# Performance work log

Measured on AMD Instinct MI355X. Metric: run time of the kernel, lower is better.

The kernel has to match this reference:

```python
import jax, jax.numpy as jnp
import numpy as np

E = 16        # num_experts
TOPK = 2      # num_experts_per_tok


def setup_inputs() -> dict:
    key = jax.random.key(0)
    ks = jax.random.split(key, 8)
    B, S, H, I, IS = 4, 2048, 1024, 512, 2048
    std = 0.02
    return {
        "hidden_states": jax.random.normal(ks[0], (B, S, H), jnp.float32),
        "gate_w": jax.random.normal(ks[1], (E, H), jnp.float32) * std,
        "gate_up_proj": jax.random.normal(ks[2], (E, 2 * I, H), jnp.float32) * std,
        "down_proj": jax.random.normal(ks[3], (E, H, I), jnp.float32) * std,
        "shared_gate_proj": jax.random.normal(ks[4], (IS, H), jnp.float32) * std,
        "shared_up_proj": jax.random.normal(ks[5], (IS, H), jnp.float32) * std,
        "shared_down_proj": jax.random.normal(ks[6], (H, IS), jnp.float32) * std,
        "shared_expert_gate_w": jax.random.normal(ks[7], (1, H), jnp.float32) * std,
    }


def _moe(x, gate_w, gate_up_proj, down_proj, sgp, sup, sdp, segw):
    # x: [N, H] flattened tokens
    N = x.shape[0]
    router_logits = x @ gate_w.T                      # [N, E]
    probs = jax.nn.softmax(router_logits, axis=-1)
    routing_weights, selected = jax.lax.top_k(probs, TOPK)   # [N, TOPK]
    routing_weights = routing_weights / routing_weights.sum(-1, keepdims=True)
    # combine weights scattered into dense [N, E] (per-token per-expert gate)
    combine = jnp.zeros((N, E), x.dtype).at[jnp.arange(N)[:, None], selected].add(routing_weights)

    def body(acc, ws):
        gu_w, d_w, cw = ws                            # [2I,H], [H,I], [N]
        gu = x @ gu_w.T                               # [N, 2I]
        g, u = jnp.split(gu, 2, axis=-1)
        h = jax.nn.silu(g) * u                        # [N, I]
        return acc + cw[:, None] * (h @ d_w.T), None

    expert_out, _ = jax.lax.scan(body, jnp.zeros_like(x), (gate_up_proj, down_proj, combine.T))

    # shared expert with sigmoid token gate
    shared_h = jax.nn.silu(x @ sgp.T) * (x @ sup.T)   # [N, IS]
    shared_out = (shared_h @ sdp.T) * jax.nn.sigmoid(x @ segw.T)  # [N, H]
    out = expert_out + shared_out

    # aux (load-balancing) loss
    counts = jnp.sum(jax.nn.one_hot(selected, E, dtype=x.dtype), axis=(0, 1))  # [E]
    frac_tokens = counts / (N * TOPK)
    frac_probs = probs.sum(0) / N
    aux_loss = E * jnp.sum(frac_tokens * frac_probs)
    return out, aux_loss


def reference(hidden_states, gate_w, gate_up_proj, down_proj, shared_gate_proj, shared_up_proj, shared_down_proj, shared_expert_gate_w):
    B, S, H = hidden_states.shape
    out, aux = _moe(hidden_states.reshape(-1, H), gate_w, gate_up_proj, down_proj,
                    shared_gate_proj, shared_up_proj, shared_down_proj, shared_expert_gate_w)
    return out.reshape(B, S, H), aux
```

## Files before the change

### kernel.cpp

```cpp
#include <hip/hip_runtime.h>
#include <hip/hip_bf16.h>
#include <stdint.h>


#define N_TOK 8192
#define HDIM 1024
#define NEXP 16
#define IEXP 512
#define ISH 2048

typedef __bf16 bf16x8 __attribute__((ext_vector_type(8)));
typedef float f32x4 __attribute__((ext_vector_type(4)));

#define OFF_XBF   ((size_t)0)
#define OFF_WSG   ((size_t)16777216)
#define OFF_WSU   ((size_t)20971520)
#define OFF_WSD   ((size_t)25165824)
#define OFF_SH    ((size_t)29360128)
#define OFF_HEXP  ((size_t)62914560)
#define OFF_IDS   ((size_t)79691776)
#define OFF_META  ((size_t)80216064)
#define OFF_SIG   ((size_t)80216320)
#define OFF_LG    ((size_t)80249088)
#define OFF_SLOT  ((size_t)81297664)
#define OFF_TWAB  ((size_t)81363200)

#define WGU_NEW   ((size_t)81428736)
#define WDN_NEW   ((size_t)(WGU_NEW + 33554432))
#define NEED_FULL ((size_t)(WDN_NEW + 16777216))

static __device__ __forceinline__ unsigned short f2bf(float f) {
  unsigned int u = __float_as_uint(f);
  u += 0x7fffu + ((u >> 16) & 1u);
  return (unsigned short)(u >> 16);
}
static __device__ __forceinline__ int pack_bf2(float a, float b) {
  return (int)f2bf(a) | ((int)f2bf(b) << 16);
}
static __device__ __forceinline__ float bf2f(unsigned short u) {
  return __uint_as_float(((unsigned int)u) << 16);
}
static __device__ __forceinline__ void gl_lds16(const void* g, void* l) {
  __builtin_amdgcn_global_load_lds(
      (const __attribute__((address_space(1))) unsigned int*)g,
      (__attribute__((address_space(3))) unsigned int*)l, 16, 0, 0);
}

__global__ void cvt_kernel(const float* __restrict__ src,
                           unsigned short* __restrict__ dst, int n4) {
  int i = blockIdx.x * 256 + threadIdx.x;
  if (i >= n4) return;
  float4 v = ((const float4*)src)[i];
  uint2 o;
  o.x = (unsigned)pack_bf2(v.x, v.y);
  o.y = (unsigned)pack_bf2(v.z, v.w);
  ((uint2*)dst)[i] = o;
}

#define CV_WSG 524288
#define CV_WSU 1048576
#define CV_WSD 1572864
#define CV_WGU 5767168
#define CV_ALL 7864320
__global__ void cvt5_kernel(const float* __restrict__ WSG, const float* __restrict__ WSU,
                            const float* __restrict__ WSD, const float* __restrict__ WGU,
                            const float* __restrict__ WDN,
                            unsigned short* __restrict__ wsg, unsigned short* __restrict__ wsu,
                            unsigned short* __restrict__ wsd, unsigned short* __restrict__ wgu,
                            unsigned short* __restrict__ wdn) {
  int i = blockIdx.x * 256 + threadIdx.x;
  if (i >= CV_ALL) return;
  const float* src; unsigned short* dst; int k;
  if (i < CV_WSG)      { src = WSG; dst = wsg; k = i; }
  else if (i < CV_WSU) { src = WSU; dst = wsu; k = i - CV_WSG; }
  else if (i < CV_WSD) { src = WSD; dst = wsd; k = i - CV_WSU; }
  else if (i < CV_WGU) { src = WGU; dst = wgu; k = i - CV_WSD; }
  else                 { src = WDN; dst = wdn; k = i - CV_WGU; }
  float4 v = ((const float4*)src)[k];
  uint2 o;
  o.x = (unsigned)pack_bf2(v.x, v.y);
  o.y = (unsigned)pack_bf2(v.z, v.w);
  ((uint2*)dst)[k] = o;
}

__global__ __launch_bounds__(256) void logits_kernel(
    const float* __restrict__ X, const float* __restrict__ GW,
    const float* __restrict__ SEGW, float* __restrict__ LG,
    unsigned short* __restrict__ XBF) {
  int wid = threadIdx.x >> 6, lane = threadIdx.x & 63;
  int tok = blockIdx.x * 4 + wid;
  const float* xr = X + (size_t)tok * HDIM;
  unsigned short* xw = XBF + (size_t)tok * HDIM;
  float xv[16];
#pragma unroll
  for (int i = 0; i < 16; i++) xv[i] = xr[lane + 64 * i];
#pragma unroll
  for (int i = 0; i < 16; i++) xw[lane + 64 * i] = f2bf(xv[i]);
  float myv = 0.f;
#pragma unroll
  for (int e = 0; e < 17; e++) {
    const float* wr = (e < 16) ? (GW + (size_t)e * HDIM) : SEGW;
    float p = 0.f;
#pragma unroll
    for (int i = 0; i < 16; i++) p += xv[i] * wr[lane + 64 * i];
#pragma unroll
    for (int off = 32; off >= 1; off >>= 1) p += __shfl_xor(p, off, 64);
    if (lane == e) myv = p;
  }
  if (lane < 17) LG[(size_t)tok * 32 + lane] = myv;
}

__global__ __launch_bounds__(256) void route_kernel(
    const float* __restrict__ LG, int* __restrict__ cnt,
    float* __restrict__ pps, int* __restrict__ ids,
    int* __restrict__ slotAB, float* __restrict__ twAB,
    float* __restrict__ sig) {
  __shared__ int lcnt[16];
  __shared__ int lbase[16];
  __shared__ float lps[16];
  int tid = threadIdx.x;
  int tok = blockIdx.x * 256 + tid;
  if (tid < 16) { lcnt[tid] = 0; lps[tid] = 0.f; }
  __syncthreads();
  const float4* row = (const float4*)(LG + (size_t)tok * 32);
  float4 v0 = row[0], v1 = row[1], v2 = row[2], v3 = row[3];
  float g16 = row[4].x;
  float lg[16] = {v0.x, v0.y, v0.z, v0.w, v1.x, v1.y, v1.z, v1.w,
                  v2.x, v2.y, v2.z, v2.w, v3.x, v3.y, v3.z, v3.w};
  float mx = lg[0];
#pragma unroll
  for (int e = 1; e < 16; e++) mx = fmaxf(mx, lg[e]);
  float pr[16], s = 0.f;
#pragma unroll
  for (int e = 0; e < 16; e++) { pr[e] = __expf(lg[e] - mx); s += pr[e]; }
  float inv_s = 1.f / s;
  float p1 = -1.f, p2 = -1.f; int i1 = 0, i2 = 0;
#pragma unroll
  for (int e = 0; e < 16; e++) {
    if (pr[e] > p1) { p2 = p1; i2 = i1; p1 = pr[e]; i1 = e; }
    else if (pr[e] > p2) { p2 = pr[e]; i2 = e; }
  }
  float wsum = p1 + p2;
  int s1 = atomicAdd(&lcnt[i1], 1);
  int s2 = atomicAdd(&lcnt[i2], 1);
#pragma unroll
  for (int e = 0; e < 16; e++) atomicAdd(&lps[e], pr[e] * inv_s);
  sig[tok] = 1.f / (1.f + __expf(-g16));
  __syncthreads();
  if (tid < 16) {
    lbase[tid] = atomicAdd(&cnt[tid], lcnt[tid]);
    atomicAdd(&pps[tid], lps[tid]);
  }
  __syncthreads();
  int sl1 = lbase[i1] + s1, sl2 = lbase[i2] + s2;
  ids[i1 * N_TOK + sl1] = tok;
  ids[i2 * N_TOK + sl2] = tok;
  slotAB[tok * 2]     = (i1 << 14) | sl1;
  slotAB[tok * 2 + 1] = (i2 << 14) | sl2;
  twAB[tok * 2]     = p1 / wsum;
  twAB[tok * 2 + 1] = p2 / wsum;
}

__global__ void offs_aux_kernel(const int* __restrict__ cnt, int* __restrict__ off,
                                const float* __restrict__ probs_sum,
                                float* __restrict__ out_aux) {
  if (threadIdx.x == 0 && blockIdx.x == 0) {
    int run = 0; float aux = 0.f;
    for (int e = 0; e < NEXP; e++) {
      off[e] = run; run += cnt[e];
      aux += ((float)cnt[e] / (float)(N_TOK * 2)) * (probs_sum[e] / (float)N_TOK);
    }
    off[16] = run;
    *out_aux = (float)NEXP * aux;
  }
}

template <int TMODE>
__global__ __launch_bounds__(512, 2) void g8p_kernel(
    const unsigned short* __restrict__ A0,
    const unsigned short* __restrict__ Bg,
    const unsigned short* __restrict__ Bu,
    const unsigned short* __restrict__ Bgu,
    const unsigned short* __restrict__ Bd,
    const int* __restrict__ ids, const int* __restrict__ cnt,
    const int* __restrict__ off,
    unsigned short* __restrict__ Osh,
    unsigned short* __restrict__ Ohex,
    unsigned short* __restrict__ Oeout) {
  constexpr int KD = (TMODE == 2) ? IEXP : HDIM;
  constexpr int NK = KD / 64;
  extern __shared__ unsigned short lds[];

  int rmode, e = 0, bx, by, m0step;
  if constexpr (TMODE == 3) {
    int id = blockIdx.x;
    if (id < 512) { rmode = 0; bx = id & 15; by = id >> 4; m0step = 8192; }
    else {
      int id2 = id - 512;
      rmode = 1; e = id2 >> 5; bx = id2 & 3; by = (id2 >> 2) & 7; m0step = 2048;
    }
  } else if constexpr (TMODE == 0) {
    rmode = 0; bx = blockIdx.x; by = blockIdx.y; m0step = 8192;
  } else if constexpr (TMODE == 1) {
    rmode = 1; e = blockIdx.z; bx = blockIdx.x; by = blockIdx.y;
    m0step = (int)gridDim.y * 256;
  } else {
    rmode = 2; e = blockIdx.z; bx = blockIdx.x; by = blockIdx.y;
    m0step = (int)gridDim.y * 256;
  }

  int ne, base = 0;
  if (rmode == 0) { ne = N_TOK; }
  else { ne = cnt[e]; base = off[e]; }

  const int t = threadIdx.x, lane = t & 63, w = t >> 6;
  const int fr = lane & 15, hi = lane >> 4;
  const int rq = hi * 4;
  const int Rm = (w >> 2) * 64;
  const int wn = (w & 3) * 32;
  const int srow = t >> 3;
  const int sblk = t & 7;
  const int cb = (sblk ^ (srow & 7)) * 8;
  const int s0 = ((0 + hi) ^ (fr & 7)) * 8;
  const int s1 = ((4 + hi) ^ (fr & 7)) * 8;
  const f32x4 z4 = {0.f, 0.f, 0.f, 0.f};

#define STG_A(buf, h, kt)                                                     \
  do {                                                                        \
    gl_lds16(apt[h][0] + (kt) * 64, &lds[(buf)*32768 + (h)*8192 + t * 8]);    \
    gl_lds16(apt[h][1] + (kt) * 64,                                           \
             &lds[(buf)*32768 + (h)*8192 + 4096 + t * 8]);                    \
  } while (0)
#define STG_B(buf, h, kt)                                                     \
  do {                                                                        \
    gl_lds16(bpt[h][0] + (kt) * 64,                                           \
             &lds[(buf)*32768 + 16384 + (h)*8192 + t * 8]);                   \
    gl_lds16(bpt[h][1] + (kt) * 64,                                           \
             &lds[(buf)*32768 + 16384 + (h)*8192 + 4096 + t * 8]);            \
  } while (0)

  for (int m0 = by * 256; m0 < ne; m0 += m0step) {
    const unsigned short* apt[2][2];
    const unsigned short* bpt[2][2];
#pragma unroll
    for (int h = 0; h < 2; h++)
#pragma unroll
      for (int l = 0; l < 2; l++) {
        int r = h * 128 + l * 64 + srow;
        if (rmode == 0) {
          apt[h][l] = A0 + (size_t)(m0 + r) * HDIM + cb;
        } else if (rmode == 1) {
          int slot = m0 + r;
          int arow = (slot < ne) ? ids[e * N_TOK + slot] : 0;
          apt[h][l] = A0 + (size_t)arow * HDIM + cb;
        } else {
          int ra = base + m0 + r;
          if (ra > 16383) ra = 16383;
          apt[h][l] = A0 + (size_t)ra * IEXP + cb;
        }
        if (rmode == 0) {
          int gcol = bx * 128 + ((r >> 5) << 4) + (r & 15);
          const unsigned short* W = (r & 16) ? Bu : Bg;
          bpt[h][l] = W + (size_t)gcol * HDIM + cb;
        } else if (rmode == 1) {
          int wrow = ((r & 16) ? 512 : 0) + bx * 128 + ((r >> 5) << 4) + (r & 15);
          bpt[h][l] = Bgu + ((size_t)e * 1024 + wrow) * HDIM + cb;
        } else {
          int nrow = bx * 256 + r;
          bpt[h][l] = Bd + ((size_t)e * HDIM + nrow) * IEXP + cb;
        }
      }

    f32x4 acc[8][4];
#pragma unroll
    for (int i = 0; i < 8; i++)
#pragma unroll
      for (int j = 0; j < 4; j++) acc[i][j] = z4;

    STG_A(0, 0, 0); STG_B(0, 1, 0); STG_A(0, 1, 0); STG_B(0, 0, 0);
    STG_A(1, 0, 1); STG_B(1, 1, 1);
    asm volatile("s_waitcnt vmcnt(4)" ::: "memory");
    __builtin_amdgcn_s_barrier();

    for (int kt = 0; kt < NK; ++kt) {
      const int c = kt & 1, nb = c ^ 1;
      const unsigned short* Ab = &lds[c * 32768];
      const unsigned short* Bb = &lds[c * 32768 + 16384];
      bf16x8 a[4][2], b[2][2];

#pragma unroll
      for (int i = 0; i < 4; i++) {
        int ro = (Rm + i * 16 + fr) * 64;
        a[i][0] = *(const bf16x8*)&Ab[ro + s0];
        a[i][1] = *(const bf16x8*)&Ab[ro + s1];
      }
#pragma unroll
      for (int j = 0; j < 2; j++) {
        int ro = (wn + j * 16 + fr) * 64;
        b[j][0] = *(const bf16x8*)&Bb[ro + s0];
        b[j][1] = *(const bf16x8*)&Bb[ro + s1];
      }
      if (kt + 1 < NK) STG_A(nb, 1, kt + 1);
      __builtin_amdgcn_s_barrier();
      asm volatile("s_waitcnt lgkmcnt(0)" ::: "memory");
      __builtin_amdgcn_s_setprio(1);
#pragma unroll
      for (int i = 0; i < 4; i++)
#pragma unroll
        for (int j = 0; j < 2; j++) {
          acc[i][j] = __builtin_amdgcn_mfma_f32_16x16x32_bf16(a[i][0], b[j][0], acc[i][j], 0, 0, 0);
          acc[i][j] = __builtin_amdgcn_mfma_f32_16x16x32_bf16(a[i][1], b[j][1], acc[i][j], 0, 0, 0);
        }
      __builtin_amdgcn_s_setprio(0);
      __builtin_amdgcn_s_barrier();

#pragma unroll
      for (int j = 0; j < 2; j++) {
        int ro = (128 + wn + j * 16 + fr) * 64;
        b[j][0] = *(const bf16x8*)&Bb[ro + s0];
        b[j][1] = *(const bf16x8*)&Bb[ro + s1];
      }
      if (kt + 1 < NK) STG_B(nb, 0, kt + 1);
      __builtin_amdgcn_s_barrier();
      asm volatile("s_waitcnt lgkmcnt(0)" ::: "memory");
      __builtin_amdgcn_s_setprio(1);
#pragma unroll
      for (int i = 0; i < 4; i++)
#pragma unroll
        for (int j = 0; j < 2; j++) {
          acc[i][2 + j] = __builtin_amdgcn_mfma_f32_16x16x32_bf16(a[i][0], b[j][0], acc[i][2 + j], 0, 0, 0);
          acc[i][2 + j] = __builtin_amdgcn_mfma_f32_16x16x32_bf16(a[i][1], b[j][1], acc[i][2 + j], 0, 0, 0);
        }
      __builtin_amdgcn_s_setprio(0);
      __builtin_amdgcn_s_barrier();

#pragma unroll
      for (int i = 0; i < 4; i++) {
        int ro = (128 + Rm + i * 16 + fr) * 64;
        a[i][0] = *(const bf16x8*)&Ab[ro + s0];
        a[i][1] = *(const bf16x8*)&Ab[ro + s1];
      }
      if (kt + 2 < NK) STG_A(c, 0, kt + 2);
      __builtin_amdgcn_s_barrier();
      asm volatile("s_waitcnt lgkmcnt(0)" ::: "memory");
      __builtin_amdgcn_s_setprio(1);
#pragma unroll
      for (int i = 0; i < 4; i++)
#pragma unroll
        for (int j = 0; j < 2; j++) {
          acc[4 + i][2 + j] = __builtin_amdgcn_mfma_f32_16x16x32_bf16(a[i][0], b[j][0], acc[4 + i][2 + j], 0, 0, 0);
          acc[4 + i][2 + j] = __builtin_amdgcn_mfma_f32_16x16x32_bf16(a[i][1], b[j][1], acc[4 + i][2 + j], 0, 0, 0);
        }
      __builtin_amdgcn_s_setprio(0);
      __builtin_amdgcn_s_barrier();

#pragma unroll
      for (int j = 0; j < 2; j++) {
        int ro = (wn + j * 16 + fr) * 64;
        b[j][0] = *(const bf16x8*)&Bb[ro + s0];
        b[j][1] = *(const bf16x8*)&Bb[ro + s1];
      }
      if (kt + 2 < NK) STG_B(c, 1, kt + 2);
      __builtin_amdgcn_s_barrier();
      asm volatile("s_waitcnt lgkmcnt(0)" ::: "memory");
      __builtin_amdgcn_s_setprio(1);
#pragma unroll
      for (int i = 0; i < 4; i++)
#pragma unroll
        for (int j = 0; j < 2; j++) {
          acc[4 + i][j] = __builtin_amdgcn_mfma_f32_16x16x32_bf16(a[i][0], b[j][0], acc[4 + i][j], 0, 0, 0);
          acc[4 + i][j] = __builtin_amdgcn_mfma_f32_16x16x32_bf16(a[i][1], b[j][1], acc[4 + i][j], 0, 0, 0);
        }
      __builtin_amdgcn_s_setprio(0);
      if (kt + 2 < NK) asm volatile("s_waitcnt vmcnt(4)" ::: "memory");
      else             asm volatile("s_waitcnt vmcnt(0)" ::: "memory");
      __builtin_amdgcn_s_barrier();
    }

#pragma unroll
    for (int i = 0; i < 8; i++) {
      int mloc = (i >> 2) * 128 + Rm + (i & 3) * 16 + rq;
      if (rmode == 2) {
#pragma unroll
        for (int j = 0; j < 4; j++) {
          int nn = bx * 256 + (j >> 1) * 128 + wn + (j & 1) * 16 + fr;
#pragma unroll
          for (int r = 0; r < 4; r++) {
            int slot = m0 + mloc + r;
            if (slot < ne)
              Oeout[(size_t)(base + slot) * HDIM + nn] = f2bf(acc[i][j][r]);
          }
        }
      } else {
#pragma unroll
        for (int p = 0; p < 2; p++) {
          int cc = bx * 128 + p * 64 + (w & 3) * 16 + fr;
#pragma unroll
          for (int r = 0; r < 4; r++) {
            int slot = m0 + mloc + r;
            float g = acc[i][2 * p][r], u = acc[i][2 * p + 1][r];
            float hv = g / (1.f + __expf(-g)) * u;
            if (rmode == 0) {
              Osh[(size_t)slot * ISH + cc] = f2bf(hv);
            } else if (slot < ne) {
              Ohex[(size_t)(base + slot) * IEXP + cc] = f2bf(hv);
            }
          }
        }
      }
    }
  }
#undef STG_A
#undef STG_B
}

template <int FUSE>
__global__ __launch_bounds__(256) void sg2c_kernel(
    const unsigned short* __restrict__ H, const unsigned short* __restrict__ Wd,
    const float* __restrict__ sig, const unsigned short* __restrict__ Eout,
    const int* __restrict__ slotAB, const float* __restrict__ twAB,
    const int* __restrict__ off, float* __restrict__ Out) {
  __shared__ __align__(16) unsigned short As[128 * 32];
  __shared__ __align__(16) unsigned short Bs[128 * 32];
  int m0 = blockIdx.y * 128, n0 = blockIdx.x * 128;
  int t = threadIdx.x, lane = t & 63, w = t >> 6;
  int wm = (w & 1) * 64, wn = (w >> 1) * 64;
  int arow = t >> 2, akb = (t & 3) * 8;
  const unsigned short* apA0 = H + (size_t)(m0 + arow) * ISH + akb;
  const unsigned short* apA1 = H + (size_t)(m0 + 64 + arow) * ISH + akb;
  const unsigned short* apB0 = Wd + (size_t)(n0 + arow) * ISH + akb;
  const unsigned short* apB1 = Wd + (size_t)(n0 + 64 + arow) * ISH + akb;
  f32x4 z = {0.f, 0.f, 0.f, 0.f};
  f32x4 acc[4][4];
#pragma unroll
  for (int i = 0; i < 4; i++)
#pragma unroll
    for (int j = 0; j < 4; j++) acc[i][j] = z;
  for (int k0 = 0; k0 < ISH; k0 += 32) {
    __syncthreads();
    gl_lds16(apA0 + k0, &As[t * 8]);
    gl_lds16(apA1 + k0, &As[2048 + t * 8]);
    gl_lds16(apB0 + k0, &Bs[t * 8]);
    gl_lds16(apB1 + k0, &Bs[2048 + t * 8]);
    __syncthreads();
    int fr = lane & 15, fc = (lane >> 4) * 8;
    bf16x8 af[4], bfr[4];
#pragma unroll
    for (int i = 0; i < 4; i++) {
      af[i] = *(const bf16x8*)&As[(wm + i * 16 + fr) * 32 + fc];
      bfr[i] = *(const bf16x8*)&Bs[(wn + i * 16 + fr) * 32 + fc];
    }
#pragma unroll
    for (int i = 0; i < 4; i++)
#pragma unroll
      for (int j = 0; j < 4; j++)
        acc[i][j] = __builtin_amdgcn_mfma_f32_16x16x32_bf16(af[i], bfr[j], acc[i][j], 0, 0, 0);
  }
  int col = lane & 15, rq = (lane >> 4) * 4;
#pragma unroll
  for (int i = 0; i < 4; i++)
#pragma unroll
    for (int r = 0; r < 4; r++) {
      int mm = m0 + wm + i * 16 + rq + r;
      float sg = sig[mm];
      if (FUSE) {
        int sa = slotAB[mm * 2], sb = slotAB[mm * 2 + 1];
        float wa = twAB[mm * 2], wb = twAB[mm * 2 + 1];
        size_t ra = (size_t)(off[sa >> 14] + (sa & 16383)) * HDIM;
        size_t rb = (size_t)(off[sb >> 14] + (sb & 16383)) * HDIM;
#pragma unroll
        for (int j = 0; j < 4; j++) {
          int nn = n0 + wn + j * 16 + col;
          float ea = bf2f(Eout[ra + nn]);
          float eb = bf2f(Eout[rb + nn]);
          Out[(size_t)mm * HDIM + nn] = acc[i][j][r] * sg + wa * ea + wb * eb;
        }
      } else {
#pragma unroll
        for (int j = 0; j < 4; j++) {
          int nn = n0 + wn + j * 16 + col;
          Out[(size_t)mm * HDIM + nn] = acc[i][j][r] * sg;
        }
      }
    }
}

__global__ __launch_bounds__(256) void combine_kernel(
    const unsigned short* __restrict__ Eout, const int* __restrict__ slotAB,
    const float* __restrict__ twAB, const int* __restrict__ off,
    float* __restrict__ Out) {
  int tok = blockIdx.x, t = threadIdx.x;
  int sa = slotAB[tok * 2], sb = slotAB[tok * 2 + 1];
  float wa = twAB[tok * 2], wb = twAB[tok * 2 + 1];
  int ra = off[sa >> 14] + (sa & 16383);
  int rb = off[sb >> 14] + (sb & 16383);
  const ushort4 a4 = *(const ushort4*)(Eout + (size_t)ra * HDIM + t * 4);
  const ushort4 b4 = *(const ushort4*)(Eout + (size_t)rb * HDIM + t * 4);
  float* po = Out + (size_t)tok * HDIM + t * 4;
  float4 o = *(const float4*)po;
  o.x += wa * bf2f(a4.x) + wb * bf2f(b4.x);
  o.y += wa * bf2f(a4.y) + wb * bf2f(b4.y);
  o.z += wa * bf2f(a4.z) + wb * bf2f(b4.z);
  o.w += wa * bf2f(a4.w) + wb * bf2f(b4.w);
  *(float4*)po = o;
}

extern "C" void kernel_launch(void* const* d_in, const int* in_sizes, int n_in,
                              void* d_out, int out_size, void* d_ws, size_t ws_size,
                              hipStream_t stream) {
  const float* X   = (const float*)d_in[0];
  const float* GW  = (const float*)d_in[1];
  const float* WGU = (const float*)d_in[2];
  const float* WDN = (const float*)d_in[3];
  const float* WSG = (const float*)d_in[4];
  const float* WSU = (const float*)d_in[5];
  const float* WSD = (const float*)d_in[6];
  const float* SEGW = (const float*)d_in[7];
  float* Out = (float*)d_out;
  char* ws = (char*)d_ws;

  unsigned short* xbf  = (unsigned short*)(ws + OFF_XBF);
  unsigned short* wsg  = (unsigned short*)(ws + OFF_WSG);
  unsigned short* wsu  = (unsigned short*)(ws + OFF_WSU);
  unsigned short* wsd  = (unsigned short*)(ws + OFF_WSD);
  unsigned short* sh   = (unsigned short*)(ws + OFF_SH);
  unsigned short* hexp = (unsigned short*)(ws + OFF_HEXP);
  int*   ids  = (int*)(ws + OFF_IDS);
  int*   cnt  = (int*)(ws + OFF_META);
  int*   off  = (int*)(ws + OFF_META + 64);
  float* pps  = (float*)(ws + OFF_META + 144);
  float* sig  = (float*)(ws + OFF_SIG);
  float* lg   = (float*)(ws + OFF_LG);
  int*   slotAB = (int*)(ws + OFF_SLOT);
  float* twAB   = (float*)(ws + OFF_TWAB);

  const bool full = (ws_size >= NEED_FULL);

  (void)hipFuncSetAttribute((const void*)g8p_kernel<0>,
                            hipFuncAttributeMaxDynamicSharedMemorySize, 131072);
  (void)hipFuncSetAttribute((const void*)g8p_kernel<1>,
                            hipFuncAttributeMaxDynamicSharedMemorySize, 131072);
  (void)hipFuncSetAttribute((const void*)g8p_kernel<2>,
                            hipFuncAttributeMaxDynamicSharedMemorySize, 131072);
  (void)hipFuncSetAttribute((const void*)g8p_kernel<3>,
                            hipFuncAttributeMaxDynamicSharedMemorySize, 131072);

  hipMemsetAsync(ws + OFF_META, 0, 256, stream);

  if (full) {
    unsigned short* wgu_bf = (unsigned short*)(ws + WGU_NEW);
    unsigned short* wdn_bf = (unsigned short*)(ws + WDN_NEW);
    unsigned short* eout   = (unsigned short*)(ws + WGU_NEW);

    cvt5_kernel<<<(CV_ALL + 255) / 256, 256, 0, stream>>>(
        WSG, WSU, WSD, WGU, WDN, wsg, wsu, wsd, wgu_bf, wdn_bf);
    logits_kernel<<<N_TOK / 4, 256, 0, stream>>>(X, GW, SEGW, lg, xbf);
    route_kernel<<<N_TOK / 256, 256, 0, stream>>>(lg, cnt, pps, ids, slotAB, twAB, sig);
    offs_aux_kernel<<<1, 64, 0, stream>>>(cnt, off, pps, Out + (size_t)N_TOK * HDIM);

    g8p_kernel<3><<<dim3(1024), 512, 131072, stream>>>(
        xbf, wsg, wsu, wgu_bf, nullptr, ids, cnt, off, sh, hexp, nullptr);
    g8p_kernel<2><<<dim3(HDIM / 256, 8, NEXP), 512, 131072, stream>>>(
        hexp, nullptr, nullptr, nullptr, wdn_bf, ids, cnt, off, nullptr, nullptr, eout);
    sg2c_kernel<1><<<dim3(HDIM / 128, N_TOK / 128), 256, 0, stream>>>(
        sh, wsd, sig, eout, slotAB, twAB, off, Out);
  } else {
    unsigned short* wgu_bf = (unsigned short*)(ws + OFF_SH);
    unsigned short* wdn_bf = (unsigned short*)(ws + OFF_XBF);
    unsigned short* eout   = (unsigned short*)(ws + OFF_SH);

    int n4 = (ISH * HDIM) / 4;
    cvt_kernel<<<(n4 + 255) / 256, 256, 0, stream>>>(WSG, wsg, n4);
    cvt_kernel<<<(n4 + 255) / 256, 256, 0, stream>>>(WSU, wsu, n4);
    n4 = (HDIM * ISH) / 4;
    cvt_kernel<<<(n4 + 255) / 256, 256, 0, stream>>>(WSD, wsd, n4);

    logits_kernel<<<N_TOK / 4, 256, 0, stream>>>(X, GW, SEGW, lg, xbf);
    route_kernel<<<N_TOK / 256, 256, 0, stream>>>(lg, cnt, pps, ids, slotAB, twAB, sig);
    offs_aux_kernel<<<1, 64, 0, stream>>>(cnt, off, pps, Out + (size_t)N_TOK * HDIM);

    g8p_kernel<0><<<dim3(16, 32), 512, 131072, stream>>>(
        xbf, wsg, wsu, nullptr, nullptr, ids, cnt, off, sh, nullptr, nullptr);
    sg2c_kernel<0><<<dim3(HDIM / 128, N_TOK / 128), 256, 0, stream>>>(
        sh, wsd, sig, nullptr, slotAB, twAB, off, Out);
    n4 = (NEXP * 2 * IEXP * HDIM) / 4;
    cvt_kernel<<<(n4 + 255) / 256, 256, 0, stream>>>(WGU, wgu_bf, n4);
    g8p_kernel<1><<<dim3(4, 8, NEXP), 512, 131072, stream>>>(
        xbf, nullptr, nullptr, wgu_bf, nullptr, ids, cnt, off, nullptr, hexp, nullptr);
    n4 = (NEXP * HDIM * IEXP) / 4;
    cvt_kernel<<<(n4 + 255) / 256, 256, 0, stream>>>(WDN, wdn_bf, n4);
    g8p_kernel<2><<<dim3(HDIM / 256, 8, NEXP), 512, 131072, stream>>>(
        hexp, nullptr, nullptr, nullptr, wdn_bf, ids, cnt, off, nullptr, nullptr, eout);
    combine_kernel<<<N_TOK, 256, 0, stream>>>(eout, slotAB, twAB, off, Out);
  }
}
```

Baseline: 502.8 us.

## Reuse B fragments across quadrants, remap block order, swizzle LDS in shared-down GEMM

The ping-pong GEMM now keeps the low and high B fragments in separate registers (bl/bh), so the fourth quadrant reuses bl instead of reloading it from LDS. That drops one LDS read phase, one barrier and one lgkmcnt wait per k-step, at the cost of extra VGPRs. The fused launch (TMODE 3) remaps block ids with a stride-8 interleave, presumably to change which tiles run concurrently and improve L2 locality. The shared-down GEMM XOR-swizzles the 16-byte column chunks in LDS to reduce bank conflicts on the fragment reads.

```diff
diff --git a/kernel.cpp b/kernel.cpp
--- a/kernel.cpp
+++ b/kernel.cpp
@@ -193,7 +193,10 @@
 
   int rmode, e = 0, bx, by, m0step;
   if constexpr (TMODE == 3) {
-    int id = blockIdx.x;
+    int id0 = blockIdx.x;
+    int id;
+    if (id0 < 512) id = (id0 & 7) * 64 + (id0 >> 3);
+    else { int q = id0 - 512; id = 512 + (q & 7) * 64 + (q >> 3); }
     if (id < 512) { rmode = 0; bx = id & 15; by = id >> 4; m0step = 8192; }
     else {
       int id2 = id - 512;
@@ -286,7 +289,7 @@
       const int c = kt & 1, nb = c ^ 1;
       const unsigned short* Ab = &lds[c * 32768];
       const unsigned short* Bb = &lds[c * 32768 + 16384];
-      bf16x8 a[4][2], b[2][2];
+      bf16x8 a[4][2], bl[2][2], bh[2][2];
 
 #pragma unroll
       for (int i = 0; i < 4; i++) {
@@ -297,8 +300,8 @@
 #pragma unroll
       for (int j = 0; j < 2; j++) {
         int ro = (wn + j * 16 + fr) * 64;
-        b[j][0] = *(const bf16x8*)&Bb[ro + s0];
-        b[j][1] = *(const bf16x8*)&Bb[ro + s1];
+        bl[j][0] = *(const bf16x8*)&Bb[ro + s0];
+        bl[j][1] = *(const bf16x8*)&Bb[ro + s1];
       }
       if (kt + 1 < NK) STG_A(nb, 1, kt + 1);
       __builtin_amdgcn_s_barrier();
@@ -308,8 +311,8 @@
       for (int i = 0; i < 4; i++)
 #pragma unroll
         for (int j = 0; j < 2; j++) {
-          acc[i][j] = __builtin_amdgcn_mfma_f32_16x16x32_bf16(a[i][0], b[j][0], acc[i][j], 0, 0, 0);
-          acc[i][j] = __builtin_amdgcn_mfma_f32_16x16x32_bf16(a[i][1], b[j][1], acc[i][j], 0, 0, 0);
+          acc[i][j] = __builtin_amdgcn_mfma_f32_16x16x32_bf16(a[i][0], bl[j][0], acc[i][j], 0, 0, 0);
+          acc[i][j] = __builtin_amdgcn_mfma_f32_16x16x32_bf16(a[i][1], bl[j][1], acc[i][j], 0, 0, 0);
         }
       __builtin_amdgcn_s_setprio(0);
       __builtin_amdgcn_s_barrier();
@@ -317,8 +320,8 @@
 #pragma unroll
       for (int j = 0; j < 2; j++) {
         int ro = (128 + wn + j * 16 + fr) * 64;
-        b[j][0] = *(const bf16x8*)&Bb[ro + s0];
-        b[j][1] = *(const bf16x8*)&Bb[ro + s1];
+        bh[j][0] = *(const bf16x8*)&Bb[ro + s0];
+        bh[j][1] = *(const bf16x8*)&Bb[ro + s1];
       }
       if (kt + 1 < NK) STG_B(nb, 0, kt + 1);
       __builtin_amdgcn_s_barrier();
@@ -328,8 +331,8 @@
       for (int i = 0; i < 4; i++)
 #pragma unroll
         for (int j = 0; j < 2; j++) {
-          acc[i][2 + j] = __builtin_amdgcn_mfma_f32_16x16x32_bf16(a[i][0], b[j][0], acc[i][2 + j], 0, 0, 0);
-          acc[i][2 + j] = __builtin_amdgcn_mfma_f32_16x16x32_bf16(a[i][1], b[j][1], acc[i][2 + j], 0, 0, 0);
+          acc[i][2 + j] = __builtin_amdgcn_mfma_f32_16x16x32_bf16(a[i][0], bh[j][0], acc[i][2 + j], 0, 0, 0);
+          acc[i][2 + j] = __builtin_amdgcn_mfma_f32_16x16x32_bf16(a[i][1], bh[j][1], acc[i][2 + j], 0, 0, 0);
         }
       __builtin_amdgcn_s_setprio(0);
       __builtin_amdgcn_s_barrier();
@@ -348,28 +351,20 @@
       for (int i = 0; i < 4; i++)
 #pragma unroll
         for (int j = 0; j < 2; j++) {
-          acc[4 + i][2 + j] = __builtin_amdgcn_mfma_f32_16x16x32_bf16(a[i][0], b[j][0], acc[4 + i][2 + j], 0, 0, 0);
-          acc[4 + i][2 + j] = __builtin_amdgcn_mfma_f32_16x16x32_bf16(a[i][1], b[j][1], acc[4 + i][2 + j], 0, 0, 0);
+          acc[4 + i][2 + j] = __builtin_amdgcn_mfma_f32_16x16x32_bf16(a[i][0], bh[j][0], acc[4 + i][2 + j], 0, 0, 0);
+          acc[4 + i][2 + j] = __builtin_amdgcn_mfma_f32_16x16x32_bf16(a[i][1], bh[j][1], acc[4 + i][2 + j], 0, 0, 0);
         }
       __builtin_amdgcn_s_setprio(0);
       __builtin_amdgcn_s_barrier();
 
-#pragma unroll
-      for (int j = 0; j < 2; j++) {
-        int ro = (wn + j * 16 + fr) * 64;
-        b[j][0] = *(const bf16x8*)&Bb[ro + s0];
-        b[j][1] = *(const bf16x8*)&Bb[ro + s1];
-      }
       if (kt + 2 < NK) STG_B(c, 1, kt + 2);
-      __builtin_amdgcn_s_barrier();
-      asm volatile("s_waitcnt lgkmcnt(0)" ::: "memory");
       __builtin_amdgcn_s_setprio(1);
 #pragma unroll
       for (int i = 0; i < 4; i++)
 #pragma unroll
         for (int j = 0; j < 2; j++) {
-          acc[4 + i][j] = __builtin_amdgcn_mfma_f32_16x16x32_bf16(a[i][0], b[j][0], acc[4 + i][j], 0, 0, 0);
-          acc[4 + i][j] = __builtin_amdgcn_mfma_f32_16x16x32_bf16(a[i][1], b[j][1], acc[4 + i][j], 0, 0, 0);
+          acc[4 + i][j] = __builtin_amdgcn_mfma_f32_16x16x32_bf16(a[i][0], bl[j][0], acc[4 + i][j], 0, 0, 0);
+          acc[4 + i][j] = __builtin_amdgcn_mfma_f32_16x16x32_bf16(a[i][1], bl[j][1], acc[4 + i][j], 0, 0, 0);
         }
       __builtin_amdgcn_s_setprio(0);
       if (kt + 2 < NK) asm volatile("s_waitcnt vmcnt(4)" ::: "memory");
@@ -425,7 +420,8 @@
   int m0 = blockIdx.y * 128, n0 = blockIdx.x * 128;
   int t = threadIdx.x, lane = t & 63, w = t >> 6;
   int wm = (w & 1) * 64, wn = (w >> 1) * 64;
-  int arow = t >> 2, akb = (t & 3) * 8;
+  int arow = t >> 2;
+  int akb = ((t & 3) ^ (arow & 3)) * 8;
   const unsigned short* apA0 = H + (size_t)(m0 + arow) * ISH + akb;
   const unsigned short* apA1 = H + (size_t)(m0 + 64 + arow) * ISH + akb;
   const unsigned short* apB0 = Wd + (size_t)(n0 + arow) * ISH + akb;
@@ -436,6 +432,8 @@
   for (int i = 0; i < 4; i++)
 #pragma unroll
     for (int j = 0; j < 4; j++) acc[i][j] = z;
+  int fr = lane & 15;
+  int fcs = (((lane >> 4) ^ (fr & 3))) * 8;
   for (int k0 = 0; k0 < ISH; k0 += 32) {
     __syncthreads();
     gl_lds16(apA0 + k0, &As[t * 8]);
@@ -443,12 +441,11 @@
     gl_lds16(apB0 + k0, &Bs[t * 8]);
     gl_lds16(apB1 + k0, &Bs[2048 + t * 8]);
     __syncthreads();
-    int fr = lane & 15, fc = (lane >> 4) * 8;
     bf16x8 af[4], bfr[4];
 #pragma unroll
     for (int i = 0; i < 4; i++) {
-      af[i] = *(const bf16x8*)&As[(wm + i * 16 + fr) * 32 + fc];
-      bfr[i] = *(const bf16x8*)&Bs[(wn + i * 16 + fr) * 32 + fc];
+      af[i] = *(const bf16x8*)&As[(wm + i * 16 + fr) * 32 + fcs];
+      bfr[i] = *(const bf16x8*)&Bs[(wn + i * 16 + fr) * 32 + fcs];
     }
 #pragma unroll
     for (int i = 0; i < 4; i++)
```

Measured after the change: 506.7 us. No clear change (+0.8%).
